# Performance work log

Measured on AMD Instinct MI355X. Metric: run time of the kernel, lower is better.

## Reference

```python
import jax, jax.numpy as jnp
import numpy as np

H = 1024      # hidden_dim
NH = 16       # num_heads
HD = H // NH  # head_dim
FF = 4096     # ff_dim
EPS = 1e-6


def layer_norm(x, gamma, beta):
    # faithful to source: unbiased std (ddof=1), divide by (std + eps)
    mean = jnp.mean(x, axis=-1, keepdims=True)
    var = jnp.sum((x - mean) ** 2, axis=-1, keepdims=True) / (x.shape[-1] - 1)
    std = jnp.sqrt(var)
    return gamma * (x - mean) / (std + EPS) + beta


def linear_mulbias(x, W, b):
    # source LinearLayer: einsum('...i,io,o->...o') -> (x @ W) * b (bias MULTIPLIES)
    return jnp.einsum('bti,io->bto', x, W) * b


def setup_inputs() -> dict:
    key = jax.random.key(0)
    ks = jax.random.split(key, 11)
    B, T = 2, 2048
    return {
        'x':      jax.random.normal(ks[0], (B, T, H), jnp.float32),
        'Wqkv':   jax.random.normal(ks[1], (H, 3 * H), jnp.float32),
        'bqkv':   jax.random.normal(ks[2], (3 * H,), jnp.float32),
        'W1':     jax.random.normal(ks[3], (H, FF), jnp.float32),
        'b1':     jax.random.normal(ks[4], (FF,), jnp.float32),
        'W2':     jax.random.normal(ks[5], (FF, H), jnp.float32),
        'b2':     jax.random.normal(ks[6], (H,), jnp.float32),
        'gamma1': jax.random.normal(ks[7], (H,), jnp.float32),
        'beta1':  jax.random.normal(ks[8], (H,), jnp.float32),
        'gamma2': jax.random.normal(ks[9], (H,), jnp.float32),
        'beta2':  jax.random.normal(ks[10], (H,), jnp.float32),
    }


def attention(x, Wqkv, bqkv):
    B, T, _ = x.shape
    qkv = linear_mulbias(x, Wqkv, bqkv)                 # [B,T,3H]
    # einops 'b t (d k h) -> k b h t d' with k=3, h=NH: last dim decomposes (d,3,h)
    qkv = qkv.reshape(B, T, HD, 3, NH)
    qkv = jnp.transpose(qkv, (3, 0, 4, 1, 2))           # [3,B,NH,T,HD]
    q, k, v = qkv[0], qkv[1], qkv[2]
    scores = jnp.einsum('bhid,bhjd->bhij', q, k) / (H ** 0.5)  # scale by full hidden_dim
    attn = jax.nn.softmax(scores, axis=-1)
    out = jnp.einsum('bhij,bhjd->bhid', attn, v)        # [B,NH,T,HD]
    return jnp.transpose(out, (0, 2, 1, 3)).reshape(B, T, H)


def reference(x, Wqkv, bqkv, W1, b1, W2, b2, gamma1, beta1, gamma2, beta2):
    # dropout is identity in eval mode
    out = layer_norm(x + attention(x, Wqkv, bqkv), gamma1, beta1)
    ffn = linear_mulbias(jnp.maximum(linear_mulbias(out, W1, b1), 0.0), W2, b2)
    out = layer_norm(out + ffn, gamma2, beta2)
    return out
```

## Files before the change

kernel.cpp:

```cpp
#include <hip/hip_runtime.h>
#include <math.h>

#define B 2
#define T 2048
#define H 1024
#define NH 16
#define HD 64
#define FF 4096
#define M_TOK (B*T)
#define LOG2E 1.4426950408889634f

typedef unsigned short u16;
typedef __attribute__((ext_vector_type(8))) short bf16x8;
typedef __attribute__((ext_vector_type(4))) float f32x4;

#define WAITBAR3  asm volatile("s_waitcnt vmcnt(3)\n\ts_barrier" ::: "memory")
#define WAITBAR4  asm volatile("s_waitcnt vmcnt(4)\n\ts_barrier" ::: "memory")
#define WAITBAR0  asm volatile("s_waitcnt vmcnt(0)\n\ts_barrier" ::: "memory")

__device__ __forceinline__ u16 f2bf(float f) {
  union { float f; unsigned u; } v; v.f = f;
  const unsigned r = (v.u + 0x7FFFu + ((v.u >> 16) & 1u)) >> 16;
  return (u16)r;
}
__device__ __forceinline__ float bf2f(u16 h) {
  union { unsigned u; float f; } v; v.u = ((unsigned)h) << 16;
  return v.f;
}
__device__ __forceinline__ unsigned cvt_pk_bf16(float lo, float hi) {
  unsigned r;
  asm("v_cvt_pk_bf16_f32 %0, %1, %2" : "=v"(r) : "v"(lo), "v"(hi));
  return r;
}
__device__ __forceinline__ float m3(float a, float b, float c) {
  return fmaxf(fmaxf(a, b), c);
}
__device__ __forceinline__ void gload16(const u16* g, u16* l) {
  __builtin_amdgcn_global_load_lds(
      (const __attribute__((address_space(1))) unsigned int*)g,
      (__attribute__((address_space(3))) unsigned int*)l, 16, 0, 0);
}

__device__ __forceinline__ int colperm(int c) {
  const int d = c / 48;
  const int rem = c - d * 48;
  return ((rem >> 4) << 10) | ((rem & 15) << 6) | d;
}

__global__ __launch_bounds__(256) void preprocess(
    const float* __restrict__ x, u16* __restrict__ xh, u16* __restrict__ xl,
    const float* __restrict__ Wqkv, u16* __restrict__ WqTh, u16* __restrict__ WqTl,
    const float* __restrict__ bqkv, float* __restrict__ bqkvP)
{
  const int bid = blockIdx.x;
  const int tid = threadIdx.x;
  if (bid == 4864) {
#pragma unroll
    for (int it = 0; it < 12; ++it) {
      const int c = it * 256 + tid;
      bqkvP[colperm(c)] = bqkv[c];
    }
    return;
  }
  if (bid < 4096) {
    const size_t i = ((size_t)bid * 256 + tid) * 4;
    const float4 v = *(const float4*)(x + i);
    union { u16 s[4]; uint2 u; } h, l;
    const float f[4] = {v.x, v.y, v.z, v.w};
#pragma unroll
    for (int j = 0; j < 4; ++j) {
      const u16 hb = f2bf(f[j]); h.s[j] = hb; l.s[j] = f2bf(f[j] - bf2f(hb));
    }
    *(uint2*)(xh + i) = h.u;
    *(uint2*)(xl + i) = l.u;
    return;
  }
  __shared__ float tile[64][69];
  const int tb = bid - 4096;
  const int K = H, N = 3*H;
  const int n0 = (tb % 48) * 64, k0 = (tb / 48) * 64;
  const int r = tid >> 4, c4 = (tid & 15) * 4;
#pragma unroll
  for (int i = 0; i < 4; ++i) {
    const float4 v = *(const float4*)(Wqkv + (size_t)(k0 + i*16 + r) * N + n0 + c4);
    tile[i*16+r][c4]   = v.x; tile[i*16+r][c4+1] = v.y;
    tile[i*16+r][c4+2] = v.z; tile[i*16+r][c4+3] = v.w;
  }
  __syncthreads();
  const int n = tid >> 2, kq = tid & 3;
  union { u16 s[8]; int4 v; } ph0, ph1, pl0, pl1;
#pragma unroll
  for (int j = 0; j < 8; ++j) {
    const float f0 = tile[kq*16 + j][n];
    const float f1 = tile[kq*16 + 8 + j][n];
    const u16 h0 = f2bf(f0), h1 = f2bf(f1);
    ph0.s[j] = h0; ph1.s[j] = h1;
    pl0.s[j] = f2bf(f0 - bf2f(h0)); pl1.s[j] = f2bf(f1 - bf2f(h1));
  }
  const int orow = colperm(n0 + n);
  u16* po = WqTh + (size_t)orow * K + k0 + kq * 16;
  *(int4*)po = ph0.v; *(int4*)(po + 8) = ph1.v;
  u16* pl = WqTl + (size_t)orow * K + k0 + kq * 16;
  *(int4*)pl = pl0.v; *(int4*)(pl + 8) = pl1.v;
}

__device__ __forceinline__ int swz(int r, int kq) {
  return r * 32 + ((kq ^ ((r >> 1) & 3)) * 8);
}

template<int RELU, int OBF>
__global__ __launch_bounds__(256) void mfma_gemm(
    const u16* __restrict__ Ah, const u16* __restrict__ Bh,
    const float* __restrict__ bias,
    float* __restrict__ Cf, u16* __restrict__ Cb,
    int M, int N, int K)
{
  __shared__ u16 lds[24576];
  const int tid = threadIdx.x;
  const int bid = blockIdx.x;
  const int xcd = bid & 7;
  const int idx = bid >> 3;
  const int row0 = (xcd * 4 + (idx & 3)) * 128;
  const int col0 = (idx >> 2) * 128;
  const int wv = tid >> 6, lane = tid & 63;
  const int wr = wv >> 1, wc = wv & 1;
  const int kq = lane >> 4, fr = lane & 15;

  f32x4 acc[4][4] = {};

#define GSTAGE(lbase, gb, rowbase, kk) do { \
    _Pragma("unroll") \
    for (int t_ = 0; t_ < 2; ++t_) { \
      const int c_ = wv * 2 + t_; \
      const int idx_ = c_ * 64 + lane; \
      const int r_ = idx_ >> 2; \
      const int kq_ = (idx_ & 3) ^ ((r_ >> 1) & 3); \
      gload16((gb) + (size_t)((rowbase) + r_) * K + (kk) + kq_ * 8, \
              &lds[(lbase) + c_ * 512]); \
    } } while (0)

  const int nk = K >> 5;
  GSTAGE(0, Ah, row0, 0);            GSTAGE(4096, Bh, col0, 0);
  GSTAGE(8192, Ah, row0, 32);        GSTAGE(8192 + 4096, Bh, col0, 32);
  WAITBAR4;
  int cslot = 0, islot = 2;
  for (int i = 0; i < nk; ++i) {
    if (i + 2 < nk) {
      const int kk = (i + 2) * 32;
      GSTAGE(islot * 8192, Ah, row0, kk);
      GSTAGE(islot * 8192 + 4096, Bh, col0, kk);
      islot = (islot == 2) ? 0 : islot + 1;
    }
    const int rb = cslot * 8192;
    bf16x8 a_h[4];
#pragma unroll
    for (int m = 0; m < 4; ++m)
      a_h[m] = *(const bf16x8*)&lds[rb + swz(wr*64 + m*16 + fr, kq)];
#pragma unroll
    for (int n = 0; n < 4; ++n) {
      const bf16x8 b_h = *(const bf16x8*)&lds[rb + 4096 + swz(wc*64 + n*16 + fr, kq)];
#pragma unroll
      for (int m = 0; m < 4; ++m)
        acc[m][n] = __builtin_amdgcn_mfma_f32_16x16x32_bf16(a_h[m], b_h, acc[m][n], 0, 0, 0);
    }
    cslot = (cslot == 2) ? 0 : cslot + 1;
    if (i + 1 < nk) { if (i + 2 < nk) WAITBAR4; else WAITBAR0; }
  }
#undef GSTAGE

  const int orow0 = row0 + wr * 64, ocol0 = col0 + wc * 64;
#pragma unroll
  for (int n = 0; n < 4; ++n) {
    const int col = ocol0 + n * 16 + fr;
    const float bs = bias[col];
#pragma unroll
    for (int m = 0; m < 4; ++m) {
      const int rbase = orow0 + m * 16 + kq * 4;
#pragma unroll
      for (int j = 0; j < 4; ++j) {
        float v = acc[m][n][j] * bs;
        if (RELU) v = fmaxf(v, 0.0f);
        const size_t off = (size_t)(rbase + j) * N + col;
        if (OBF) Cb[off] = f2bf(v); else Cf[off] = v;
      }
    }
  }
}

__global__ __launch_bounds__(256) void mfma_qkv(
    const u16* __restrict__ Ah, const u16* __restrict__ Al,
    const u16* __restrict__ Bh, const u16* __restrict__ Bl,
    const float* __restrict__ biasP,
    u16* __restrict__ Qh, u16* __restrict__ Ql,
    u16* __restrict__ Kh, u16* __restrict__ Kl, u16* __restrict__ VT,
    const float* __restrict__ W1_, u16* __restrict__ W1T_,
    const float* __restrict__ W2_, u16* __restrict__ W2T_)
{
  const int K = H;
  __shared__ u16 lds[32768];
  const int tid = threadIdx.x;
  const int bid0 = blockIdx.x;

  if (bid0 >= 768) {
    float* tile = (float*)lds;
    const float* in; u16* oh; int Kt, Nt, k0, n0;
    if (bid0 < 1792) {
      const int tb = bid0 - 768;
      in = W1_; oh = W1T_; Kt = H; Nt = FF;
      n0 = (tb & 63) * 64; k0 = (tb >> 6) * 64;
    } else {
      const int tb = bid0 - 1792;
      in = W2_; oh = W2T_; Kt = FF; Nt = H;
      n0 = (tb & 15) * 64; k0 = (tb >> 4) * 64;
    }
    const int r = tid >> 4, c4 = (tid & 15) * 4;
#pragma unroll
    for (int i = 0; i < 4; ++i) {
      const float4 v = *(const float4*)(in + (size_t)(k0 + i*16 + r) * Nt + n0 + c4);
      tile[(i*16+r)*69 + c4]     = v.x; tile[(i*16+r)*69 + c4 + 1] = v.y;
      tile[(i*16+r)*69 + c4 + 2] = v.z; tile[(i*16+r)*69 + c4 + 3] = v.w;
    }
    __syncthreads();
    const int n = tid >> 2, kqt = tid & 3;
    union { u16 s[8]; int4 v; } ph0, ph1;
#pragma unroll
    for (int j = 0; j < 8; ++j) {
      ph0.s[j] = f2bf(tile[(kqt*16 + j)*69 + n]);
      ph1.s[j] = f2bf(tile[(kqt*16 + 8 + j)*69 + n]);
    }
    u16* po = oh + (size_t)(n0 + n) * Kt + k0 + kqt * 16;
    *(int4*)po = ph0.v; *(int4*)(po + 8) = ph1.v;
    return;
  }

  const int bid = bid0;
  const int xcd = bid & 7;
  const int idx = bid >> 3;
  const int row0 = (xcd * 4 + (idx & 3)) * 128;
  const int col0 = (idx >> 2) * 128;
  const int wv = tid >> 6, lane = tid & 63;
  const int wr = wv >> 1, wc = wv & 1;
  const int kq = lane >> 4, fr = lane & 15;
  const bool isV = (col0 >= 2048);

  f32x4 acc[4][4] = {};

#define QSTAGE(lbase, gb, rowbase, kk) do { \
    _Pragma("unroll") \
    for (int t_ = 0; t_ < 2; ++t_) { \
      const int c_ = wv * 2 + t_; \
      const int idx_ = c_ * 64 + lane; \
      const int r_ = idx_ >> 2; \
      const int kq_ = (idx_ & 3) ^ ((r_ >> 1) & 3); \
      gload16((gb) + (size_t)((rowbase) + r_) * K + (kk) + kq_ * 8, \
              &lds[(lbase) + c_ * 512]); \
    } } while (0)

  if (isV) {
    const int nk = K >> 5;
    QSTAGE(0, Ah, row0, 0);            QSTAGE(4096, Bh, col0, 0);
    QSTAGE(8192, Ah, row0, 32);        QSTAGE(8192 + 4096, Bh, col0, 32);
    WAITBAR4;
    int cslot = 0, islot = 2;
    for (int i = 0; i < nk; ++i) {
      if (i + 2 < nk) {
        const int kk = (i + 2) * 32;
        QSTAGE(islot * 8192, Ah, row0, kk);
        QSTAGE(islot * 8192 + 4096, Bh, col0, kk);
        islot = (islot == 2) ? 0 : islot + 1;
      }
      const int rb = cslot * 8192;
      bf16x8 a_h[4];
#pragma unroll
      for (int m = 0; m < 4; ++m)
        a_h[m] = *(const bf16x8*)&lds[rb + swz(wr*64 + m*16 + fr, kq)];
#pragma unroll
      for (int n = 0; n < 4; ++n) {
        const bf16x8 b_h = *(const bf16x8*)&lds[rb + 4096 + swz(wc*64 + n*16 + fr, kq)];
#pragma unroll
        for (int m = 0; m < 4; ++m)
          acc[m][n] = __builtin_amdgcn_mfma_f32_16x16x32_bf16(a_h[m], b_h, acc[m][n], 0, 0, 0);
      }
      cslot = (cslot == 2) ? 0 : cslot + 1;
      if (i + 1 < nk) { if (i + 2 < nk) WAITBAR4; else WAITBAR0; }
    }
    __syncthreads();

    const int ocol0 = col0 + wc * 64;
#pragma unroll
    for (int n = 0; n < 4; ++n) {
      const int dc = wc * 64 + n * 16 + fr;
      const float bs = biasP[ocol0 + n * 16 + fr];
#pragma unroll
      for (int m = 0; m < 4; ++m) {
        const int trb = wr * 64 + m * 16 + kq * 4;
#pragma unroll
        for (int j = 0; j < 4; ++j)
          lds[dc * 132 + trb + j] = f2bf(acc[m][n][j] * bs);
      }
    }
    __syncthreads();
    const int dr_ = tid >> 1, half = tid & 1;
    const int hh = ((col0 >> 6) & 15) + (dr_ >> 6);
    const int d = dr_ & 63;
    const int b = row0 >> 11, t0r = row0 & (T - 1);
    u16* dstp = VT + (((size_t)(b * NH + hh)) * HD + d) * T + t0r + half * 64;
    const int sbase = dr_ * 132 + half * 64;
#pragma unroll
    for (int q = 0; q < 8; ++q) {
      union { uint2 u2[2]; int4 v; } pkv;
      pkv.u2[0] = *(const uint2*)&lds[sbase + q * 8];
      pkv.u2[1] = *(const uint2*)&lds[sbase + q * 8 + 4];
      *(int4*)(dstp + q * 8) = pkv.v;
    }
    return;
  }

  QSTAGE(0, Ah, row0, 0);
  QSTAGE(4096, Bh, col0, 0);
  QSTAGE(8192, Al, row0, 0);
  QSTAGE(12288, Bl, col0, 0);
  __syncthreads();

  int cur = 0;
  for (int k0 = 0; k0 < K; k0 += 32) {
    const int nxt = cur ^ 1;
    if (k0 + 32 < K) {
      QSTAGE(nxt*16384, Ah, row0, k0 + 32);
      QSTAGE(nxt*16384 + 4096, Bh, col0, k0 + 32);
      QSTAGE(nxt*16384 + 8192, Al, row0, k0 + 32);
      QSTAGE(nxt*16384 + 12288, Bl, col0, k0 + 32);
    }
    const int rb = cur * 16384;
    bf16x8 a_h[4], a_l[4];
#pragma unroll
    for (int m = 0; m < 4; ++m) {
      a_h[m] = *(const bf16x8*)&lds[rb + swz(wr*64 + m*16 + fr, kq)];
      a_l[m] = *(const bf16x8*)&lds[rb + 8192 + swz(wr*64 + m*16 + fr, kq)];
    }
#pragma unroll
    for (int n = 0; n < 4; ++n) {
      const bf16x8 b_h = *(const bf16x8*)&lds[rb + 4096 + swz(wc*64 + n*16 + fr, kq)];
      const bf16x8 b_l = *(const bf16x8*)&lds[rb + 12288 + swz(wc*64 + n*16 + fr, kq)];
#pragma unroll
      for (int m = 0; m < 4; ++m) {
        acc[m][n] = __builtin_amdgcn_mfma_f32_16x16x32_bf16(a_h[m], b_h, acc[m][n], 0, 0, 0);
        acc[m][n] = __builtin_amdgcn_mfma_f32_16x16x32_bf16(a_h[m], b_l, acc[m][n], 0, 0, 0);
        acc[m][n] = __builtin_amdgcn_mfma_f32_16x16x32_bf16(a_l[m], b_h, acc[m][n], 0, 0, 0);
      }
    }
    __syncthreads();
    cur = nxt;
  }
#undef QSTAGE

  const float qscale = LOG2E / 32.0f;
  const int orow0 = row0 + wr * 64, ocol0 = col0 + wc * 64;
  const int kcls = col0 >> 10;
#pragma unroll
  for (int n = 0; n < 4; ++n) {
    const int colp = ocol0 + n * 16 + fr;
    const int d = colp & 63, hh = (colp >> 6) & 15;
    const float bs = biasP[colp];
#pragma unroll
    for (int m = 0; m < 4; ++m) {
      const int rbase = orow0 + m * 16 + kq * 4;
#pragma unroll
      for (int j = 0; j < 4; ++j) {
        const int row = rbase + j;
        const int b = row >> 11, t = row & (T - 1);
        const size_t dst = (((size_t)(b * NH + hh)) * T + t) * HD + d;
        float v = acc[m][n][j] * bs;
        if (kcls == 0) {
          v *= qscale;
          const u16 hb = f2bf(v);
          Qh[dst] = hb; Ql[dst] = f2bf(v - bf2f(hb));
        } else {
          const u16 hb = f2bf(v);
          Kh[dst] = hb; Kl[dst] = f2bf(v - bf2f(hb));
        }
      }
    }
  }
}

__global__ __launch_bounds__(512, 2) void mfma_ffn2(
    const u16* __restrict__ Ah, const u16* __restrict__ Bh,
    const u16* __restrict__ Res, const float* __restrict__ bias,
    u16* __restrict__ Y)
{
  const int N = H, K = FF;
  __shared__ u16 lds[2 * 24576];
  const int tid = threadIdx.x;
  const int bid = blockIdx.x;
  const int xcd = bid & 7;
  const int idx = bid >> 3;
  const int row0 = (xcd * 4 + (idx & 3)) * 128;
  const int col0 = (idx >> 2) * 128;
  const int wv8 = tid >> 6, lane = tid & 63;
  const int grp = wv8 >> 2, wv = wv8 & 3;
  const int wr = wv >> 1, wc = wv & 1;
  const int kq = lane >> 4, fr = lane & 15;
  const int kb = grp * (K >> 1);
  u16* gl = &lds[grp * 24576];

  f32x4 acc[4][4] = {};

#define GSTAGE2(lbase, gb, rowbase, kk) do { \
    _Pragma("unroll") \
    for (int t_ = 0; t_ < 2; ++t_) { \
      const int c_ = wv * 2 + t_; \
      const int idx_ = c_ * 64 + lane; \
      const int r_ = idx_ >> 2; \
      const int kq_ = (idx_ & 3) ^ ((r_ >> 1) & 3); \
      gload16((gb) + (size_t)((rowbase) + r_) * K + (kk) + kq_ * 8, \
              &gl[(lbase) + c_ * 512]); \
    } } while (0)

  const int nk = (K >> 1) >> 5;
  GSTAGE2(0, Ah, row0, kb);            GSTAGE2(4096, Bh, col0, kb);
  GSTAGE2(8192, Ah, row0, kb + 32);    GSTAGE2(8192 + 4096, Bh, col0, kb + 32);
  WAITBAR4;
  int cslot = 0, islot = 2;
  for (int i = 0; i < nk; ++i) {
    if (i + 2 < nk) {
      const int kk = kb + (i + 2) * 32;
      GSTAGE2(islot * 8192, Ah, row0, kk);
      GSTAGE2(islot * 8192 + 4096, Bh, col0, kk);
      islot = (islot == 2) ? 0 : islot + 1;
    }
    const int rb = cslot * 8192;
    bf16x8 a_h[4];
#pragma unroll
    for (int m = 0; m < 4; ++m)
      a_h[m] = *(const bf16x8*)&gl[rb + swz(wr*64 + m*16 + fr, kq)];
#pragma unroll
    for (int n = 0; n < 4; ++n) {
      const bf16x8 b_h = *(const bf16x8*)&gl[rb + 4096 + swz(wc*64 + n*16 + fr, kq)];
#pragma unroll
      for (int m = 0; m < 4; ++m)
        acc[m][n] = __builtin_amdgcn_mfma_f32_16x16x32_bf16(a_h[m], b_h, acc[m][n], 0, 0, 0);
    }
    cslot = (cslot == 2) ? 0 : cslot + 1;
    if (i + 1 < nk) { if (i + 2 < nk) WAITBAR4; else WAITBAR0; }
  }
#undef GSTAGE2

  __syncthreads();
  float* fm = (float*)lds;
  const int base = wv * 4096;
  if (grp == 1) {
#pragma unroll
    for (int m = 0; m < 4; ++m)
#pragma unroll
      for (int n = 0; n < 4; ++n)
        *(f32x4*)&fm[base + (m*4 + n)*256 + lane*4] = acc[m][n];
  }
  __syncthreads();
  if (grp == 0) {
    const int orow0 = row0 + wr * 64, ocol0 = col0 + wc * 64;
#pragma unroll
    for (int n = 0; n < 4; ++n) {
      const int col = ocol0 + n * 16 + fr;
      const float bs = bias[col];
#pragma unroll
      for (int m = 0; m < 4; ++m) {
        const f32x4 ob = *(const f32x4*)&fm[base + (m*4 + n)*256 + lane*4];
        const int rbase = orow0 + m * 16 + kq * 4;
#pragma unroll
        for (int j = 0; j < 4; ++j) {
          const size_t off = (size_t)(rbase + j) * N + col;
          Y[off] = f2bf(bf2f(Res[off]) + (acc[m][n][j] + ob[j]) * bs);
        }
      }
    }
  }
}

__device__ __forceinline__ int sigma_k(int r) {
  return ((r >> 5) << 5) | (((r >> 2) & 3) << 3) | (((r >> 4) & 1) << 2) | (r & 3);
}

__global__ __launch_bounds__(512, 4) void flash_attn_mfma(
    const u16* __restrict__ Qh, const u16* __restrict__ Ql,
    const u16* __restrict__ Kh, const u16* __restrict__ Kl,
    const u16* __restrict__ VT, float* __restrict__ Out)
{
  __shared__ u16 sm[3 * 12288];
  const int i = blockIdx.x;
  const int slot = i >> 3;
  const int bh = (i & 7) * 4 + (slot >> 4);
  const int row0 = (slot & 15) * 128;
  const int b = bh >> 4, h = bh & 15;
  const int tid = threadIdx.x, wave = tid >> 6, lane = tid & 63;
  const int fr = lane & 15, kq = lane >> 4;

  bf16x8 qh[2], ql[2];
  const size_t qoff = ((size_t)bh * T + row0 + wave*16 + fr) * HD + kq*8;
#pragma unroll
  for (int ks = 0; ks < 2; ++ks) {
    qh[ks] = *(const bf16x8*)(Qh + qoff + ks*32);
    ql[ks] = *(const bf16x8*)(Ql + qoff + ks*32);
  }

  bf16x8 ones8;
#pragma unroll
  for (int z = 0; z < 8; ++z) ones8[z] = (short)0x3F80;

  f32x4 o[4] = {};
  f32x4 oex = {};
  float m_ = -1e30f;

  const int c_ = wave;
  const int r0_ = c_ * 8 + (lane >> 3), s_ = lane & 7;
  const int cd0 = s_ ^ (r0_ & 7);
  const int k0_ = sigma_k(r0_);
  const u16* pKh0 = Kh + ((size_t)bh*T + k0_)*HD + cd0*8;
  const u16* pKl0 = Kl + ((size_t)bh*T + k0_)*HD + cd0*8;
  const u16* pV0  = VT + ((size_t)bh*HD + r0_)*T + cd0*8;

#define FSTAGE(sb) do { \
    gload16(pKh0, &sm[(sb) + c_*512]); \
    gload16(pKl0, &sm[(sb) + 4096 + c_*512]); \
    gload16(pV0,  &sm[(sb) + 8192 + c_*512]); \
    pKh0 += 64*HD; pKl0 += 64*HD; pV0 += 64; \
  } while (0)

  FSTAGE(0);
  FSTAGE(12288);
  WAITBAR3;
  int cslot = 0, islot = 2;

  const int NT = T / 64;
  for (int t = 0; t < NT; ++t) {
    if (t + 2 < NT) {
      FSTAGE(islot * 12288);
      islot = (islot == 2) ? 0 : islot + 1;
    }
    const u16* smb = &sm[cslot * 12288];

    f32x4 s[4] = {};
    __builtin_amdgcn_s_setprio(1);
#pragma unroll
    for (int ks = 0; ks < 2; ++ks) {
#pragma unroll
      for (int n = 0; n < 4; ++n) {
        const int kr = n * 16 + fr;
        const int sl = ((ks*4 + kq) ^ (kr & 7)) * 8;
        const bf16x8 kh_ = *(const bf16x8*)&smb[kr*64 + sl];
        const bf16x8 kl_ = *(const bf16x8*)&smb[4096 + kr*64 + sl];
        s[n] = __builtin_amdgcn_mfma_f32_16x16x32_bf16(kh_, qh[ks], s[n], 0, 0, 0);
        s[n] = __builtin_amdgcn_mfma_f32_16x16x32_bf16(kl_, qh[ks], s[n], 0, 0, 0);
        s[n] = __builtin_amdgcn_mfma_f32_16x16x32_bf16(kh_, ql[ks], s[n], 0, 0, 0);
      }
    }
    __builtin_amdgcn_s_setprio(0);

    const float g0 = m3(s[0][0], s[0][1], s[0][2]);
    const float g1 = m3(s[0][3], s[1][0], s[1][1]);
    const float g2 = m3(s[1][2], s[1][3], s[2][0]);
    const float g3 = m3(s[2][1], s[2][2], s[2][3]);
    const float g4 = m3(s[3][0], s[3][1], s[3][2]);
    float mx = fmaxf(m3(g0, g1, g2), m3(g3, g4, s[3][3]));
    mx = fmaxf(mx, __shfl_xor(mx, 16));
    mx = fmaxf(mx, __shfl_xor(mx, 32));
    if (!__all(mx <= m_ + 8.0f)) {
      const float mn = fmaxf(m_, mx);
      const float fsc = exp2f(m_ - mn);
      m_ = mn;
#pragma unroll
      for (int n = 0; n < 4; ++n) {
        o[n][0] *= fsc; o[n][1] *= fsc;
        o[n][2] *= fsc; o[n][3] *= fsc;
      }
      oex[0] *= fsc; oex[1] *= fsc; oex[2] *= fsc; oex[3] *= fsc;
    }

    float p[4][4];
#pragma unroll
    for (int n = 0; n < 4; ++n)
#pragma unroll
      for (int jj = 0; jj < 4; ++jj)
        p[n][jj] = exp2f(s[n][jj] - m_);

    unsigned pk[4][2];
#pragma unroll
    for (int n = 0; n < 4; ++n) {
      pk[n][0] = cvt_pk_bf16(p[n][0], p[n][1]);
      pk[n][1] = cvt_pk_bf16(p[n][2], p[n][3]);
    }

    __builtin_amdgcn_s_setprio(1);
#pragma unroll
    for (int ks = 0; ks < 2; ++ks) {
      union { unsigned u[4]; bf16x8 v; } pb;
      pb.u[0] = pk[2*ks][0];   pb.u[1] = pk[2*ks][1];
      pb.u[2] = pk[2*ks+1][0]; pb.u[3] = pk[2*ks+1][1];
#pragma unroll
      for (int n = 0; n < 4; ++n) {
        const int dr = n * 16 + fr;
        const bf16x8 vf = *(const bf16x8*)&smb[8192 + dr*64 + (((ks*4 + kq) ^ (dr & 7)) * 8)];
        o[n] = __builtin_amdgcn_mfma_f32_16x16x32_bf16(vf, pb.v, o[n], 0, 0, 0);
      }
      oex = __builtin_amdgcn_mfma_f32_16x16x32_bf16(ones8, pb.v, oex, 0, 0, 0);
    }
    __builtin_amdgcn_s_setprio(0);

    cslot = (cslot == 2) ? 0 : cslot + 1;
    if (t + 1 < NT) { if (t + 2 < NT) WAITBAR3; else WAITBAR0; }
  }
#undef FSTAGE

  {
    const float inv = 1.0f / oex[0];
    const size_t qrow = (size_t)b * T + row0 + wave*16 + fr;
#pragma unroll
    for (int n = 0; n < 4; ++n) {
      float4 ov;
      ov.x = o[n][0] * inv; ov.y = o[n][1] * inv;
      ov.z = o[n][2] * inv; ov.w = o[n][3] * inv;
      *(float4*)(Out + qrow * H + h * HD + n * 16 + kq * 4) = ov;
    }
  }
}

__global__ __launch_bounds__(256) void ln_residual(
    const float* __restrict__ A, const float* __restrict__ Bz,
    const float* __restrict__ gamma, const float* __restrict__ beta,
    u16* __restrict__ obf)
{
  const int row = blockIdx.x, tid = threadIdx.x;
  const int wave = tid >> 6, lane = tid & 63;
  const size_t off = (size_t)row * H + tid * 4;
  const float4 av = *(const float4*)(A + off);
  const float4 bv = *(const float4*)(Bz + off);
  float4 y; y.x = av.x + bv.x; y.y = av.y + bv.y; y.z = av.z + bv.z; y.w = av.w + bv.w;
  float s  = y.x + y.y + y.z + y.w;
  float ss = y.x*y.x + y.y*y.y + y.z*y.z + y.w*y.w;
#pragma unroll
  for (int o = 32; o >= 1; o >>= 1) { s += __shfl_xor(s, o); ss += __shfl_xor(ss, o); }
  __shared__ float red[2][4];
  if (lane == 0) { red[0][wave] = s; red[1][wave] = ss; }
  __syncthreads();
  s  = red[0][0] + red[0][1] + red[0][2] + red[0][3];
  ss = red[1][0] + red[1][1] + red[1][2] + red[1][3];
  const float mean = s * (1.0f / (float)H);
  float var = (ss - (float)H * mean * mean) * (1.0f / (float)(H - 1));
  var = fmaxf(var, 0.0f);
  const float inv = 1.0f / (sqrtf(var) + 1e-6f);
  const float4 gv = *(const float4*)(gamma + tid * 4);
  const float4 be = *(const float4*)(beta + tid * 4);
  float4 o;
  o.x = gv.x * (y.x - mean) * inv + be.x;
  o.y = gv.y * (y.y - mean) * inv + be.y;
  o.z = gv.z * (y.z - mean) * inv + be.z;
  o.w = gv.w * (y.w - mean) * inv + be.w;
  union { u16 s[4]; uint2 u; } pk;
  pk.s[0] = f2bf(o.x); pk.s[1] = f2bf(o.y); pk.s[2] = f2bf(o.z); pk.s[3] = f2bf(o.w);
  *(uint2*)(obf + off) = pk.u;
}

__global__ __launch_bounds__(256) void ln_only(
    const u16* __restrict__ Yv,
    const float* __restrict__ gamma, const float* __restrict__ beta,
    float* __restrict__ out)
{
  const int row = blockIdx.x, tid = threadIdx.x;
  const int wave = tid >> 6, lane = tid & 63;
  const size_t off = (size_t)row * H + tid * 4;
  union { uint2 u; u16 s[4]; } yu;
  yu.u = *(const uint2*)(Yv + off);
  float4 y;
  y.x = bf2f(yu.s[0]); y.y = bf2f(yu.s[1]);
  y.z = bf2f(yu.s[2]); y.w = bf2f(yu.s[3]);
  float s  = y.x + y.y + y.z + y.w;
  float ss = y.x*y.x + y.y*y.y + y.z*y.z + y.w*y.w;
#pragma unroll
  for (int o = 32; o >= 1; o >>= 1) { s += __shfl_xor(s, o); ss += __shfl_xor(ss, o); }
  __shared__ float red[2][4];
  if (lane == 0) { red[0][wave] = s; red[1][wave] = ss; }
  __syncthreads();
  s  = red[0][0] + red[0][1] + red[0][2] + red[0][3];
  ss = red[1][0] + red[1][1] + red[1][2] + red[1][3];
  const float mean = s * (1.0f / (float)H);
  float var = (ss - (float)H * mean * mean) * (1.0f / (float)(H - 1));
  var = fmaxf(var, 0.0f);
  const float inv = 1.0f / (sqrtf(var) + 1e-6f);
  const float4 gv = *(const float4*)(gamma + tid * 4);
  const float4 be = *(const float4*)(beta + tid * 4);
  float4 o;
  o.x = gv.x * (y.x - mean) * inv + be.x;
  o.y = gv.y * (y.y - mean) * inv + be.y;
  o.z = gv.z * (y.z - mean) * inv + be.z;
  o.w = gv.w * (y.w - mean) * inv + be.w;
  *(float4*)(out + off) = o;
}

extern "C" void kernel_launch(void* const* d_in, const int* in_sizes, int n_in,
                              void* d_out, int out_size, void* d_ws, size_t ws_size,
                              hipStream_t stream)
{
  const float* x    = (const float*)d_in[0];
  const float* Wqkv = (const float*)d_in[1];
  const float* bqkv = (const float*)d_in[2];
  const float* W1   = (const float*)d_in[3];
  const float* b1   = (const float*)d_in[4];
  const float* W2   = (const float*)d_in[5];
  const float* b2   = (const float*)d_in[6];
  const float* g1   = (const float*)d_in[7];
  const float* be1  = (const float*)d_in[8];
  const float* g2   = (const float*)d_in[9];
  const float* be2  = (const float*)d_in[10];
  float* out = (float*)d_out;
  char* w = (char*)d_ws;

  u16*   Qh    = (u16*)  (w + 0);
  u16*   Ql    = (u16*)  (w + 8388608);
  u16*   Khb   = (u16*)  (w + 16777216);
  u16*   Klb   = (u16*)  (w + 25165824);
  u16*   VTb   = (u16*)  (w + 41943040);
  u16*   h1b   = (u16*)  (w + 0);
  u16*   xh    = (u16*)  (w + 52428800);
  u16*   xl    = (u16*)  (w + 60817408);
  u16*   WqTh  = (u16*)  (w + 69206016);
  u16*   WqTl  = (u16*)  (w + 75497472);
  float* attn  = (float*)(w + 102760448);
  u16*   Yb    = (u16*)  (w + 102760448);
  u16*   W1T   = (u16*)  (w + 119537664);
  u16*   W2T   = (u16*)  (w + 127926272);
  u16*   ln1b  = (u16*)  (w + 136314880);
  float* bqkvP = (float*)(w + 144703488);

  preprocess<<<4865, 256, 0, stream>>>(x, xh, xl, Wqkv, WqTh, WqTl,
                                       bqkv, bqkvP);
  mfma_qkv<<<2816, 256, 0, stream>>>(xh, xl, WqTh, WqTl, bqkvP,
                                     Qh, Ql, Khb, Klb, VTb,
                                     W1, W1T, W2, W2T);
  flash_attn_mfma<<<512, 512, 0, stream>>>(Qh, Ql, Khb, Klb, VTb, attn);
  ln_residual<<<M_TOK, 256, 0, stream>>>(x, attn, g1, be1, ln1b);
  mfma_gemm<1,1><<<32 * 32, 256, 0, stream>>>(ln1b, W1T, b1,
                                              nullptr, h1b, M_TOK, FF, H);
  mfma_ffn2<<<256, 512, 0, stream>>>(h1b, W2T, ln1b, b2, Yb);
  ln_only<<<M_TOK, 256, 0, stream>>>(Yb, g2, be2, out);
}
```

Baseline: 258.5 us.

## Replace split-K FFN2 GEMM with 64x128 tiles over 512 blocks

The FFN2 GEMM used 128x128 output tiles with two 4-wave groups splitting K, then reduced the partial sums through LDS. It now uses 64x128 tiles, 4 waves per block and the full K per block, launched as 512 blocks of 256 threads. This removes the cross-group LDS reduction and its barriers and doubles the block count. In exchange each block runs twice as many K iterations serially, and the smaller tile loads B data from global memory more times overall.

```diff
diff --git a/kernel.cpp b/kernel.cpp
--- a/kernel.cpp
+++ b/kernel.cpp
@@ -384,94 +384,80 @@
   }
 }
 
-__global__ __launch_bounds__(512, 2) void mfma_ffn2(
+__global__ __launch_bounds__(256) void mfma_ffn2(
     const u16* __restrict__ Ah, const u16* __restrict__ Bh,
     const u16* __restrict__ Res, const float* __restrict__ bias,
     u16* __restrict__ Y)
 {
   const int N = H, K = FF;
-  __shared__ u16 lds[2 * 24576];
+  __shared__ u16 lds[3 * 6144];
   const int tid = threadIdx.x;
   const int bid = blockIdx.x;
   const int xcd = bid & 7;
   const int idx = bid >> 3;
-  const int row0 = (xcd * 4 + (idx & 3)) * 128;
-  const int col0 = (idx >> 2) * 128;
-  const int wv8 = tid >> 6, lane = tid & 63;
-  const int grp = wv8 >> 2, wv = wv8 & 3;
+  const int row0 = (xcd * 8 + (idx & 7)) * 64;
+  const int col0 = (idx >> 3) * 128;
+  const int wv = tid >> 6, lane = tid & 63;
   const int wr = wv >> 1, wc = wv & 1;
   const int kq = lane >> 4, fr = lane & 15;
-  const int kb = grp * (K >> 1);
-  u16* gl = &lds[grp * 24576];
-
-  f32x4 acc[4][4] = {};
-
-#define GSTAGE2(lbase, gb, rowbase, kk) do { \
+
+  f32x4 acc[2][4] = {};
+
+#define FSTG(sb, kk) do { \
+    { const int idx_ = wv * 64 + lane; \
+      const int r_ = idx_ >> 2; \
+      const int kq_ = (idx_ & 3) ^ ((r_ >> 1) & 3); \
+      gload16(Ah + (size_t)(row0 + r_) * K + (kk) + kq_ * 8, \
+              &lds[(sb) + wv * 512]); } \
     _Pragma("unroll") \
     for (int t_ = 0; t_ < 2; ++t_) { \
       const int c_ = wv * 2 + t_; \
       const int idx_ = c_ * 64 + lane; \
       const int r_ = idx_ >> 2; \
       const int kq_ = (idx_ & 3) ^ ((r_ >> 1) & 3); \
-      gload16((gb) + (size_t)((rowbase) + r_) * K + (kk) + kq_ * 8, \
-              &gl[(lbase) + c_ * 512]); \
+      gload16(Bh + (size_t)(col0 + r_) * K + (kk) + kq_ * 8, \
+              &lds[(sb) + 2048 + c_ * 512]); \
     } } while (0)
 
-  const int nk = (K >> 1) >> 5;
-  GSTAGE2(0, Ah, row0, kb);            GSTAGE2(4096, Bh, col0, kb);
-  GSTAGE2(8192, Ah, row0, kb + 32);    GSTAGE2(8192 + 4096, Bh, col0, kb + 32);
-  WAITBAR4;
+  const int nk = K >> 5;
+  FSTG(0, 0);
+  FSTG(6144, 32);
+  WAITBAR3;
   int cslot = 0, islot = 2;
   for (int i = 0; i < nk; ++i) {
     if (i + 2 < nk) {
-      const int kk = kb + (i + 2) * 32;
-      GSTAGE2(islot * 8192, Ah, row0, kk);
-      GSTAGE2(islot * 8192 + 4096, Bh, col0, kk);
+      FSTG(islot * 6144, (i + 2) * 32);
       islot = (islot == 2) ? 0 : islot + 1;
     }
-    const int rb = cslot * 8192;
-    bf16x8 a_h[4];
-#pragma unroll
-    for (int m = 0; m < 4; ++m)
-      a_h[m] = *(const bf16x8*)&gl[rb + swz(wr*64 + m*16 + fr, kq)];
+    const int rb = cslot * 6144;
+    bf16x8 a_h[2];
+#pragma unroll
+    for (int m = 0; m < 2; ++m)
+      a_h[m] = *(const bf16x8*)&lds[rb + swz(wr*32 + m*16 + fr, kq)];
 #pragma unroll
     for (int n = 0; n < 4; ++n) {
-      const bf16x8 b_h = *(const bf16x8*)&gl[rb + 4096 + swz(wc*64 + n*16 + fr, kq)];
-#pragma unroll
-      for (int m = 0; m < 4; ++m)
+      const bf16x8 b_h = *(const bf16x8*)&lds[rb + 2048 + swz(wc*64 + n*16 + fr, kq)];
+#pragma unroll
+      for (int m = 0; m < 2; ++m)
         acc[m][n] = __builtin_amdgcn_mfma_f32_16x16x32_bf16(a_h[m], b_h, acc[m][n], 0, 0, 0);
     }
     cslot = (cslot == 2) ? 0 : cslot + 1;
-    if (i + 1 < nk) { if (i + 2 < nk) WAITBAR4; else WAITBAR0; }
-  }
-#undef GSTAGE2
-
-  __syncthreads();
-  float* fm = (float*)lds;
-  const int base = wv * 4096;
-  if (grp == 1) {
-#pragma unroll
-    for (int m = 0; m < 4; ++m)
-#pragma unroll
-      for (int n = 0; n < 4; ++n)
-        *(f32x4*)&fm[base + (m*4 + n)*256 + lane*4] = acc[m][n];
-  }
-  __syncthreads();
-  if (grp == 0) {
-    const int orow0 = row0 + wr * 64, ocol0 = col0 + wc * 64;
-#pragma unroll
-    for (int n = 0; n < 4; ++n) {
-      const int col = ocol0 + n * 16 + fr;
-      const float bs = bias[col];
-#pragma unroll
-      for (int m = 0; m < 4; ++m) {
-        const f32x4 ob = *(const f32x4*)&fm[base + (m*4 + n)*256 + lane*4];
-        const int rbase = orow0 + m * 16 + kq * 4;
-#pragma unroll
-        for (int j = 0; j < 4; ++j) {
-          const size_t off = (size_t)(rbase + j) * N + col;
-          Y[off] = f2bf(bf2f(Res[off]) + (acc[m][n][j] + ob[j]) * bs);
-        }
+    if (i + 1 < nk) { if (i + 2 < nk) WAITBAR3; else WAITBAR0; }
+  }
+#undef FSTG
+
+  const int orow0 = row0 + wr * 32, ocol0 = col0 + wc * 64;
+#pragma unroll
+  for (int n = 0; n < 4; ++n) {
+    const int col = ocol0 + n * 16 + fr;
+    const float bs = bias[col];
+#pragma unroll
+    for (int m = 0; m < 2; ++m) {
+      const int rbase = orow0 + m * 16 + kq * 4;
+#pragma unroll
+      for (int j = 0; j < 4; ++j) {
+        const size_t off = (size_t)(rbase + j) * N + col;
+        Y[off] = f2bf(bf2f(Res[off]) + acc[m][n][j] * bs);
       }
     }
   }
@@ -740,6 +726,6 @@
   ln_residual<<<M_TOK, 256, 0, stream>>>(x, attn, g1, be1, ln1b);
   mfma_gemm<1,1><<<32 * 32, 256, 0, stream>>>(ln1b, W1T, b1,
                                               nullptr, h1b, M_TOK, FF, H);
-  mfma_ffn2<<<256, 512, 0, stream>>>(h1b, W2T, ln1b, b2, Yb);
+  mfma_ffn2<<<512, 256, 0, stream>>>(h1b, W2T, ln1b, b2, Yb);
   ln_only<<<M_TOK, 256, 0, stream>>>(Yb, g2, be2, out);
 }
```

Measured after the change: 270.7 us. 1.05x slower.
